# Optimization experiments

Measured on AMD Instinct MI355X. Metric: run time of the kernel, lower is better.

Reference implementation:

```python
import jax, jax.numpy as jnp
import numpy as np

TAU = 0.5
EPS = 1e-12  # F.normalize default eps


def _projection(z, fc1_w, fc1_b, fc2_w, fc2_b):
    h = jax.nn.elu(z @ fc1_w.T + fc1_b)
    return h @ fc2_w.T + fc2_b


def _normalize(z):
    n = jnp.linalg.norm(z, axis=1, keepdims=True)
    return z / jnp.maximum(n, EPS)


def _semi_loss(h1, h2):
    z1 = _normalize(h1)
    z2 = _normalize(h2)
    refl_sim = jnp.exp((z1 @ z1.T) / TAU)      # [N, N]
    between_sim = jnp.exp((z1 @ z2.T) / TAU)   # [N, N]
    pos = jnp.diagonal(between_sim)
    denom = refl_sim.sum(axis=1) + between_sim.sum(axis=1) - jnp.diagonal(refl_sim)
    return -jnp.log(pos / denom)


def setup_inputs() -> dict:
    key = jax.random.key(0)
    k1, k2, k3, k4 = jax.random.split(key, 4)
    N, H, P = 8192, 512, 512
    s1 = 1.0 / np.sqrt(H)
    s2 = 1.0 / np.sqrt(P)
    return {
        "z1": jax.random.normal(k1, (N, H), jnp.float32),
        "z2": jax.random.normal(k2, (N, H), jnp.float32),
        "fc1_w": jax.random.normal(k3, (P, H), jnp.float32) * s1,
        "fc1_b": jnp.zeros((P,), jnp.float32),
        "fc2_w": jax.random.normal(k4, (H, P), jnp.float32) * s2,
        "fc2_b": jnp.zeros((H,), jnp.float32),
    }


def reference(z1, z2, fc1_w, fc1_b, fc2_w, fc2_b):
    h1 = _projection(z1, fc1_w, fc1_b, fc2_w, fc2_b)
    h2 = _projection(z2, fc1_w, fc1_b, fc2_w, fc2_b)
    l1 = _semi_loss(h1, h2)
    l2 = _semi_loss(h2, h1)
    ret = (l1 + l2) * 0.5
    return ret.mean()
```

## Files before the change

### kernel.cpp

```cpp
#include <hip/hip_runtime.h>
#include <math.h>

typedef __attribute__((ext_vector_type(8))) __bf16 bf16x8;
typedef __attribute__((ext_vector_type(4))) float f32x4;
typedef __attribute__((ext_vector_type(16))) float f32x16;
typedef __attribute__((ext_vector_type(8))) unsigned short u16x8;
typedef __attribute__((ext_vector_type(8))) int i32x8;

#define GAS(p) ((const __attribute__((address_space(1))) void*)(p))
#define LAS(p) ((__attribute__((address_space(3))) void*)(p))

__device__ __forceinline__ unsigned short f2bf(float f) {
  union { float f; unsigned int u; } v; v.f = f;
  unsigned int r = (v.u + 0x7FFFu + ((v.u >> 16) & 1u)) >> 16;
  return (unsigned short)r;
}
__device__ __forceinline__ float bf2f(unsigned short b) {
  union { unsigned int u; float f; } v; v.u = ((unsigned int)b) << 16;
  return v.f;
}

__global__ __launch_bounds__(256) void cast_all_kernel(
    const float* __restrict__ z1, const float* __restrict__ z2,
    const float* __restrict__ w1, const float* __restrict__ w2,
    unsigned short* __restrict__ z1b, unsigned short* __restrict__ z2b,
    unsigned short* __restrict__ w1b, unsigned short* __restrict__ w2b) {
  int b = blockIdx.x;
  const float* in; unsigned short* out; int base;
  if (b < 4096)       { in = z1; out = z1b; base = b; }
  else if (b < 8192)  { in = z2; out = z2b; base = b - 4096; }
  else if (b < 8448)  { in = w1; out = w1b; base = b - 8192; }
  else                { in = w2; out = w2b; base = b - 8448; }
  int i = (base * 256 + threadIdx.x) * 4;
  float4 v = *(const float4*)(in + i);
  ushort4 o;
  o.x = f2bf(v.x); o.y = f2bf(v.y); o.z = f2bf(v.z); o.w = f2bf(v.w);
  *(ushort4*)(out + i) = o;
}

__device__ __forceinline__ void gemm_tile_512_db(
    const unsigned short* __restrict__ A, const unsigned short* __restrict__ B,
    int m0, int n0, unsigned short* lA, unsigned short* lB, f32x4 acc[4][4]) {
  constexpr int K = 512;
  const int tid  = threadIdx.x;
  const int wave = tid >> 6;
  const int lane = tid & 63;
  const int quad = lane >> 4;
  const int l16  = lane & 15;
  const int wrow = (wave & 1) * 64;
  const int wcol = (wave >> 1) * 64;

  const f32x4 zero = {0.f, 0.f, 0.f, 0.f};
#pragma unroll
  for (int i = 0; i < 4; ++i)
#pragma unroll
    for (int j = 0; j < 4; ++j) acc[i][j] = zero;

  const int e0 = wave * 1024 + lane * 8;
  const int r0 = e0 >> 5, c0 = e0 & 31;
  const int e1 = e0 + 512;
  const int r1 = e1 >> 5, c1 = e1 & 31;

  const unsigned short* Ag0 = A + (size_t)(m0 + r0) * K + c0;
  const unsigned short* Ag1 = A + (size_t)(m0 + r1) * K + c1;
  const unsigned short* Bg0 = B + (size_t)(n0 + r0) * K + c0;
  const unsigned short* Bg1 = B + (size_t)(n0 + r1) * K + c1;

  __builtin_amdgcn_global_load_lds(GAS(Ag0), LAS(&lA[e0]), 16, 0, 0);
  __builtin_amdgcn_global_load_lds(GAS(Ag1), LAS(&lA[e1]), 16, 0, 0);
  __builtin_amdgcn_global_load_lds(GAS(Bg0), LAS(&lB[e0]), 16, 0, 0);
  __builtin_amdgcn_global_load_lds(GAS(Bg1), LAS(&lB[e1]), 16, 0, 0);
  __syncthreads();

  for (int kt = 0; kt < 16; ++kt) {
    const int cur = (kt & 1) * 4096;
    if (kt < 15) {
      const int nxt = 4096 - cur;
      const int ko = (kt + 1) * 32;
      __builtin_amdgcn_global_load_lds(GAS(Ag0 + ko), LAS(&lA[nxt + e0]), 16, 0, 0);
      __builtin_amdgcn_global_load_lds(GAS(Ag1 + ko), LAS(&lA[nxt + e1]), 16, 0, 0);
      __builtin_amdgcn_global_load_lds(GAS(Bg0 + ko), LAS(&lB[nxt + e0]), 16, 0, 0);
      __builtin_amdgcn_global_load_lds(GAS(Bg1 + ko), LAS(&lB[nxt + e1]), 16, 0, 0);
    }
    bf16x8 af[4], bfr[4];
#pragma unroll
    for (int i = 0; i < 4; ++i) {
      af[i]  = *(const bf16x8*)&lA[cur + (wrow + i * 16 + l16) * 32 + quad * 8];
      bfr[i] = *(const bf16x8*)&lB[cur + (wcol + i * 16 + l16) * 32 + quad * 8];
    }
#pragma unroll
    for (int mi = 0; mi < 4; ++mi)
#pragma unroll
      for (int ni = 0; ni < 4; ++ni)
        acc[mi][ni] = __builtin_amdgcn_mfma_f32_16x16x32_bf16(
            af[mi], bfr[ni], acc[mi][ni], 0, 0, 0);
    __syncthreads();
  }
}

template<int EPI>
__global__ __launch_bounds__(256)
void proj_kernel(const unsigned short* __restrict__ A1,
                 const unsigned short* __restrict__ A2,
                 const unsigned short* __restrict__ W,
                 const float* __restrict__ bias,
                 unsigned short* __restrict__ C1,
                 unsigned short* __restrict__ C2) {
  __shared__ unsigned short lA[2 * 128 * 32];
  __shared__ unsigned short lB[2 * 128 * 32];
  const int b = blockIdx.x;
  const int which = b >> 8;
  const int r = b & 255;
  const int n0 = (r & 3) * 128;
  const int m0 = (r >> 2) * 128;
  const unsigned short* A = which ? A2 : A1;
  unsigned short* C = which ? C2 : C1;

  f32x4 acc[4][4];
  gemm_tile_512_db(A, W, m0, n0, lA, lB, acc);

  const int lane = threadIdx.x & 63;
  const int wave = threadIdx.x >> 6;
  const int quad = lane >> 4;
  const int l16  = lane & 15;
  const int wrow = (wave & 1) * 64;
  const int wcol = (wave >> 1) * 64;

#pragma unroll
  for (int ni = 0; ni < 4; ++ni) {
    const int c = n0 + wcol + ni * 16 + l16;
    const float bv = bias[c];
#pragma unroll
    for (int mi = 0; mi < 4; ++mi) {
      const int rbase = m0 + wrow + mi * 16 + quad * 4;
#pragma unroll
      for (int rr = 0; rr < 4; ++rr) {
        float v = acc[mi][ni][rr] + bv;
        if constexpr (EPI == 0) v = (v > 0.f) ? v : expm1f(v);
        C[(size_t)(rbase + rr) * 512 + c] = f2bf(v);
      }
    }
  }
}

__global__ __launch_bounds__(256, 3)
void gram_kernel(const unsigned char* __restrict__ q1,
                 const unsigned char* __restrict__ q2,
                 float* __restrict__ d11, float* __restrict__ d22,
                 float* __restrict__ d12r, float* __restrict__ d12c) {
  __shared__ unsigned char lA[32768];

  const int b = blockIdx.x;
  const unsigned char *Abase, *Bbase;
  float *rptr, *cptr;
  int r, g, cnt;
  bool cross;
  if (b < 2176) {
    const bool first = (b < 1088);
    int j = first ? b : b - 1088;
    int q = (int)((sqrtf((float)j + 1.f) - 1.f) * 0.5f);
    while (4 * (q + 1) * (q + 2) <= j) ++q;
    while (4 * q * (q + 1) > j) --q;
    const int w = j - 4 * q * (q + 1);
    const int s = w / (q + 1);
    g = w - s * (q + 1);
    r = 8 * q + s;
    const unsigned char* h = first ? q1 : q2;
    Abase = h; Bbase = h;
    rptr = first ? d11 : d22; cptr = rptr;
    cnt = min(2, (r >> 2) + 1 - 2 * g);
    cross = false;
  } else {
    const int j = b - 2176;
    g = j >> 7; r = j & 127;
    Abase = q1; Bbase = q2;
    rptr = d12r; cptr = d12c;
    cnt = 2; cross = true;
  }

  const int tid  = threadIdx.x;
  const int wave = tid >> 6;
  const int lane = tid & 63;
  const int half = lane >> 5;
  const int l31  = lane & 31;
  const int lfo  = half * 1024 + l31 * 16;

  {
    const unsigned char* Asrc = Abase + (size_t)r * 32768 + wave * 8192 + lane * 16;
    unsigned char* Adst = lA + wave * 8192 + lane * 16;
#pragma unroll
    for (int i = 0; i < 8; ++i)
      __builtin_amdgcn_global_load_lds(GAS(Asrc + i * 1024),
                                       LAS(Adst + i * 1024), 16, 0, 0);
  }
  __syncthreads();

  union frag { i32x8 v; int4 h[2]; };

  float rs[2][16];
#pragma unroll
  for (int mi = 0; mi < 2; ++mi)
#pragma unroll
    for (int rr = 0; rr < 16; ++rr) rs[mi][rr] = 0.f;

  const int d = r & 3;
  for (int t = 0; t < cnt; ++t) {
    const int c = 2 * g + t;
    const bool diagST = (!cross) && (c == (r >> 2));
    if (diagST && wave > d) break;
    const unsigned char* B0 = Bbase + (size_t)(8 * c + 2 * wave) * 16384 + lfo;
    const unsigned char* B1 = B0 + 16384;

    f32x16 acc[2][2];
#pragma unroll
    for (int i = 0; i < 2; ++i)
#pragma unroll
      for (int jj = 0; jj < 2; ++jj)
#pragma unroll
        for (int rr = 0; rr < 16; ++rr) acc[i][jj][rr] = 0.f;

#pragma unroll
    for (int KT = 0; KT < 4; ++KT) {
#pragma unroll
      for (int ktl = 0; ktl < 2; ++ktl) {
        const int ko = KT * 4096 + ktl * 2048;
        frag fa[2], fb[2];
        fb[0].h[0] = *(const int4*)(B0 + ko);
        fb[0].h[1] = *(const int4*)(B0 + ko + 512);
        fb[1].h[0] = *(const int4*)(B1 + ko);
        fb[1].h[1] = *(const int4*)(B1 + ko + 512);
#pragma unroll
        for (int i = 0; i < 2; ++i) {
          const int oa = i * 16384 + ko + lfo;
          fa[i].h[0] = *(const int4*)&lA[oa];
          fa[i].h[1] = *(const int4*)&lA[oa + 512];
        }
#pragma unroll
        for (int mi = 0; mi < 2; ++mi)
#pragma unroll
          for (int ni = 0; ni < 2; ++ni)
            acc[mi][ni] = __builtin_amdgcn_mfma_scale_f32_32x32x64_f8f6f4(
                fa[mi].v, fb[ni].v, acc[mi][ni],
                0, 0,
                0, 0x7F7F7F7F,
                0, 0x7F7F7F7F);
      }
    }

    float cs[2] = {0.f, 0.f};
#pragma unroll
    for (int mi = 0; mi < 2; ++mi)
#pragma unroll
      for (int ni = 0; ni < 2; ++ni)
#pragma unroll
        for (int rr = 0; rr < 16; ++rr) {
          float v = exp2f(2.8853900817779268f * acc[mi][ni][rr]);
          rs[mi][rr] += v;
          cs[ni] += v;
        }
    if (!(diagST && wave == d)) {
#pragma unroll
      for (int ni = 0; ni < 2; ++ni) {
        float v = cs[ni] + __shfl_xor(cs[ni], 32, 64);
        if (half == 0)
          atomicAdd(&cptr[c * 256 + wave * 64 + ni * 32 + l31], v);
      }
    }
  }

#pragma unroll
  for (int mi = 0; mi < 2; ++mi) {
#pragma unroll
    for (int dd = 1; dd < 32; dd <<= 1) {
#pragma unroll
      for (int rr = 0; rr < 16; ++rr) rs[mi][rr] += __shfl_xor(rs[mi][rr], dd, 64);
    }
    if (l31 == 0) {
      const int mb = r * 64 + mi * 32;
#pragma unroll
      for (int rr = 0; rr < 16; ++rr) {
        const int row = mb + (rr & 3) + 8 * (rr >> 2) + 4 * half;
        atomicAdd(&rptr[row], rs[mi][rr]);
      }
    }
  }
}

__global__ __launch_bounds__(256)
void norm_diag_kernel(const unsigned short* __restrict__ h1,
                      const unsigned short* __restrict__ h2,
                      unsigned char* __restrict__ q1,
                      unsigned char* __restrict__ q2,
                      float* __restrict__ cdiag) {
  const int wave = threadIdx.x >> 6, lane = threadIdx.x & 63;
  const int row = blockIdx.x * 4 + wave;
  const u16x8 u1 = *(const u16x8*)(h1 + (size_t)row * 512 + lane * 8);
  const u16x8 u2 = *(const u16x8*)(h2 + (size_t)row * 512 + lane * 8);
  float f1[8], f2[8], ss1 = 0.f, ss2 = 0.f;
#pragma unroll
  for (int j = 0; j < 8; ++j) {
    f1[j] = bf2f(u1[j]); ss1 += f1[j] * f1[j];
    f2[j] = bf2f(u2[j]); ss2 += f2[j] * f2[j];
  }
#pragma unroll
  for (int d = 1; d < 64; d <<= 1) {
    ss1 += __shfl_xor(ss1, d, 64);
    ss2 += __shfl_xor(ss2, d, 64);
  }
  const float inv1 = 1.0f / fmaxf(sqrtf(ss1), 1e-12f);
  const float inv2 = 1.0f / fmaxf(sqrtf(ss2), 1e-12f);
  float a[8], bb[8];
  float dot = 0.f;
#pragma unroll
  for (int j = 0; j < 8; ++j) {
    a[j] = f1[j] * inv1; bb[j] = f2[j] * inv2;
    dot += a[j] * bb[j];
  }
  int lo1 = __builtin_amdgcn_cvt_pk_fp8_f32(a[0], a[1], 0, false);
  lo1 = __builtin_amdgcn_cvt_pk_fp8_f32(a[2], a[3], lo1, true);
  int hi1 = __builtin_amdgcn_cvt_pk_fp8_f32(a[4], a[5], 0, false);
  hi1 = __builtin_amdgcn_cvt_pk_fp8_f32(a[6], a[7], hi1, true);
  int lo2 = __builtin_amdgcn_cvt_pk_fp8_f32(bb[0], bb[1], 0, false);
  lo2 = __builtin_amdgcn_cvt_pk_fp8_f32(bb[2], bb[3], lo2, true);
  int hi2 = __builtin_amdgcn_cvt_pk_fp8_f32(bb[4], bb[5], 0, false);
  hi2 = __builtin_amdgcn_cvt_pk_fp8_f32(bb[6], bb[7], hi2, true);

  const int c0 = lane * 8;
  const size_t dst = (size_t)(row >> 5) * 16384 + (c0 >> 6) * 2048
                   + ((c0 >> 4) & 3) * 512 + (row & 31) * 16 + (c0 & 15);
  *(int2*)(q1 + dst) = make_int2(lo1, hi1);
  *(int2*)(q2 + dst) = make_int2(lo2, hi2);
#pragma unroll
  for (int d = 1; d < 64; d <<= 1) dot += __shfl_xor(dot, d, 64);
  if (lane == 0) cdiag[row] = dot;
}

__global__ __launch_bounds__(256)
void finalize_kernel(const float* __restrict__ d11, const float* __restrict__ d22,
                     const float* __restrict__ d12r, const float* __restrict__ d12c,
                     const float* __restrict__ cdiag, float* __restrict__ out) {
  const float e2 = 7.38905609893065f;
  float s = 0.f;
  for (int i = threadIdx.x; i < 8192; i += 256) {
    const float den1 = d11[i] + d12r[i] - e2;
    const float den2 = d22[i] + d12c[i] - e2;
    s += -2.0f * cdiag[i] + 0.5f * (logf(den1) + logf(den2));
  }
#pragma unroll
  for (int d = 1; d < 64; d <<= 1) s += __shfl_xor(s, d, 64);
  __shared__ float sm[4];
  if ((threadIdx.x & 63) == 0) sm[threadIdx.x >> 6] = s;
  __syncthreads();
  if (threadIdx.x == 0) out[0] = (sm[0] + sm[1] + sm[2] + sm[3]) * (1.0f / 8192.0f);
}

extern "C" void kernel_launch(void* const* d_in, const int* in_sizes, int n_in,
                              void* d_out, int out_size, void* d_ws, size_t ws_size,
                              hipStream_t stream) {
  const float* z1 = (const float*)d_in[0];
  const float* z2 = (const float*)d_in[1];
  const float* w1 = (const float*)d_in[2];
  const float* b1 = (const float*)d_in[3];
  const float* w2 = (const float*)d_in[4];
  const float* b2 = (const float*)d_in[5];
  float* out = (float*)d_out;

  const int N = 8192, D = 512;
  char* ws = (char*)d_ws;
  auto alloc = [&](size_t bytes) {
    char* p = ws; ws += (bytes + 255) & ~(size_t)255; return p;
  };
  unsigned short* z1b = (unsigned short*)alloc((size_t)N * D * 2);
  unsigned short* z2b = (unsigned short*)alloc((size_t)N * D * 2);
  unsigned short* g1  = (unsigned short*)alloc((size_t)N * D * 2);
  unsigned short* g2  = (unsigned short*)alloc((size_t)N * D * 2);
  unsigned short* w1b = (unsigned short*)alloc((size_t)D * D * 2);
  unsigned short* w2b = (unsigned short*)alloc((size_t)D * D * 2);
  float* sums  = (float*)alloc((size_t)4 * N * sizeof(float));
  float* cdiag = (float*)alloc((size_t)N * sizeof(float));
  float* d11 = sums, *d22 = sums + N, *d12r = sums + 2 * N, *d12c = sums + 3 * N;
  unsigned short* h1 = z1b;
  unsigned short* h2 = z2b;
  unsigned char* q1 = (unsigned char*)g1;
  unsigned char* q2 = (unsigned char*)g2;

  hipMemsetAsync(sums, 0, (size_t)4 * N * sizeof(float), stream);

  cast_all_kernel<<<dim3(8704), 256, 0, stream>>>(z1, z2, w1, w2, z1b, z2b, w1b, w2b);
  proj_kernel<0><<<dim3(512), 256, 0, stream>>>(z1b, z2b, w1b, b1, g1, g2);
  proj_kernel<1><<<dim3(512), 256, 0, stream>>>(g1, g2, w2b, b2, h1, h2);
  norm_diag_kernel<<<dim3(N / 4), 256, 0, stream>>>(h1, h2, q1, q2, cdiag);
  gram_kernel<<<dim3(4224), 256, 0, stream>>>(q1, q2, d11, d22, d12r, d12c);
  finalize_kernel<<<1, 256, 0, stream>>>(d11, d22, d12r, d12c, cdiag, out);
}
```

Before: 272.3 us.

## Enlarge gram kernel tiles to 128-row A blocks with 8 waves per block

The Gram/exp-sum kernel now uses 512-thread blocks that stage a 128-row FP8 A tile (64KB LDS) and split waves into a 2x4 row/column grid, halving the block count. The triangular-tile index mapping and the diagonal-tile masking logic are rewritten for the new tile shape. The intent is to double reuse of each B fragment loaded from global memory across two A row groups and to cut per-block setup and atomic overhead. The cost is more LDS per block and therefore lower occupancy, plus coarser load balancing on the triangular work.

```diff
diff --git a/kernel.cpp b/kernel.cpp
--- a/kernel.cpp
+++ b/kernel.cpp
@@ -143,55 +143,58 @@
   }
 }
 
-__global__ __launch_bounds__(256, 3)
+__global__ __launch_bounds__(512, 4)
 void gram_kernel(const unsigned char* __restrict__ q1,
                  const unsigned char* __restrict__ q2,
                  float* __restrict__ d11, float* __restrict__ d22,
                  float* __restrict__ d12r, float* __restrict__ d12c) {
-  __shared__ unsigned char lA[32768];
+  __shared__ unsigned char lA[65536];
 
   const int b = blockIdx.x;
   const unsigned char *Abase, *Bbase;
   float *rptr, *cptr;
   int r, g, cnt;
   bool cross;
-  if (b < 2176) {
-    const bool first = (b < 1088);
-    int j = first ? b : b - 1088;
-    int q = (int)((sqrtf((float)j + 1.f) - 1.f) * 0.5f);
-    while (4 * (q + 1) * (q + 2) <= j) ++q;
-    while (4 * q * (q + 1) > j) --q;
-    const int w = j - 4 * q * (q + 1);
-    const int s = w / (q + 1);
-    g = w - s * (q + 1);
-    r = 8 * q + s;
+  if (b < 1088) {
+    const bool first = (b < 544);
+    int j = first ? b : b - 544;
+    int p = (int)((sqrtf(2.f * j + 1.f) - 1.f) * 0.5f);
+    while (2 * (p + 1) * (p + 2) <= j) ++p;
+    while (2 * p * (p + 1) > j) --p;
+    const int w = j - 2 * p * (p + 1);
+    const int dr = w / (p + 1);
+    g = w - dr * (p + 1);
+    r = 4 * p + dr;
     const unsigned char* h = first ? q1 : q2;
     Abase = h; Bbase = h;
     rptr = first ? d11 : d22; cptr = rptr;
-    cnt = min(2, (r >> 2) + 1 - 2 * g);
+    cnt = min(2, ((r >> 1) + 1) - 2 * g);
     cross = false;
   } else {
-    const int j = b - 2176;
-    g = j >> 7; r = j & 127;
+    const int j = b - 1088;
+    g = j >> 6; r = j & 63;
     Abase = q1; Bbase = q2;
     rptr = d12r; cptr = d12c;
     cnt = 2; cross = true;
   }
 
   const int tid  = threadIdx.x;
-  const int wave = tid >> 6;
+  const int wv   = tid >> 6;
   const int lane = tid & 63;
   const int half = lane >> 5;
   const int l31  = lane & 31;
+  const int rw   = wv & 1;
+  const int cw   = wv >> 1;
+  const int pa0  = rw * 2;
   const int lfo  = half * 1024 + l31 * 16;
 
   {
-    const unsigned char* Asrc = Abase + (size_t)r * 32768 + wave * 8192 + lane * 16;
-    unsigned char* Adst = lA + wave * 8192 + lane * 16;
+    const unsigned char* Asrc = Abase + (size_t)r * 65536 + tid * 16;
+    unsigned char* Adst = lA + tid * 16;
 #pragma unroll
     for (int i = 0; i < 8; ++i)
-      __builtin_amdgcn_global_load_lds(GAS(Asrc + i * 1024),
-                                       LAS(Adst + i * 1024), 16, 0, 0);
+      __builtin_amdgcn_global_load_lds(GAS(Asrc + i * 8192),
+                                       LAS(Adst + i * 8192), 16, 0, 0);
   }
   __syncthreads();
 
@@ -203,12 +206,22 @@
 #pragma unroll
     for (int rr = 0; rr < 16; ++rr) rs[mi][rr] = 0.f;
 
-  const int d = r & 3;
+  const int rhalf = r & 1;
   for (int t = 0; t < cnt; ++t) {
-    const int c = 2 * g + t;
-    const bool diagST = (!cross) && (c == (r >> 2));
-    if (diagST && wave > d) break;
-    const unsigned char* B0 = Bbase + (size_t)(8 * c + 2 * wave) * 16384 + lfo;
+    const int ct = 2 * g + t;
+    const bool diagST = (!cross) && (ct == (r >> 1));
+    int mode = 0;
+    if (diagST) {
+      const int cw2 = cw >> 1, cwl = cw & 1;
+      if (cw2 > rhalf) mode = 2;
+      else if (cw2 == rhalf) {
+        if (rw < cwl) mode = 2;
+        else if (rw == cwl) mode = 1;
+      }
+    }
+    if (mode == 2) continue;
+
+    const unsigned char* B0 = Bbase + (size_t)(8 * ct + 2 * cw) * 16384 + lfo;
     const unsigned char* B1 = B0 + 16384;
 
     f32x16 acc[2][2];
@@ -231,7 +244,7 @@
         fb[1].h[1] = *(const int4*)(B1 + ko + 512);
 #pragma unroll
         for (int i = 0; i < 2; ++i) {
-          const int oa = i * 16384 + ko + lfo;
+          const int oa = (pa0 + i) * 16384 + ko + lfo;
           fa[i].h[0] = *(const int4*)&lA[oa];
           fa[i].h[1] = *(const int4*)&lA[oa + 512];
         }
@@ -258,12 +271,12 @@
           rs[mi][rr] += v;
           cs[ni] += v;
         }
-    if (!(diagST && wave == d)) {
+    if (mode == 0) {
 #pragma unroll
       for (int ni = 0; ni < 2; ++ni) {
         float v = cs[ni] + __shfl_xor(cs[ni], 32, 64);
         if (half == 0)
-          atomicAdd(&cptr[c * 256 + wave * 64 + ni * 32 + l31], v);
+          atomicAdd(&cptr[ct * 256 + cw * 64 + ni * 32 + l31], v);
       }
     }
   }
@@ -276,7 +289,7 @@
       for (int rr = 0; rr < 16; ++rr) rs[mi][rr] += __shfl_xor(rs[mi][rr], dd, 64);
     }
     if (l31 == 0) {
-      const int mb = r * 64 + mi * 32;
+      const int mb = r * 128 + rw * 64 + mi * 32;
 #pragma unroll
       for (int rr = 0; rr < 16; ++rr) {
         const int row = mb + (rr & 3) + 8 * (rr >> 2) + 4 * half;
@@ -390,6 +403,6 @@
   proj_kernel<0><<<dim3(512), 256, 0, stream>>>(z1b, z2b, w1b, b1, g1, g2);
   proj_kernel<1><<<dim3(512), 256, 0, stream>>>(g1, g2, w2b, b2, h1, h2);
   norm_diag_kernel<<<dim3(N / 4), 256, 0, stream>>>(h1, h2, q1, q2, cdiag);
-  gram_kernel<<<dim3(4224), 256, 0, stream>>>(q1, q2, d11, d22, d12r, d12c);
+  gram_kernel<<<dim3(2112), 512, 0, stream>>>(q1, q2, d11, d22, d12r, d12c);
   finalize_kernel<<<1, 256, 0, stream>>>(d11, d22, d12r, d12c, cdiag, out);
 }
```

Result: slower. 294.7 us (+8.2%).
